# Performance work log

Measured on AMD Instinct MI355X. Metric: run time of the kernel, lower is better.

Reference implementation:

```python
import jax, jax.numpy as jnp
import numpy as np

MULT_CLASS = 6  # int(1/0.2) + 1
EPS = 1e-4


def setup_inputs() -> dict:
    key = jax.random.key(0)
    ks = jax.random.split(key, 8)
    bs, C, M, D = 16384, 10000, MULT_CLASS, 256
    return {
        "data": jax.random.normal(ks[0], (bs, D), dtype=jnp.float32),
        "source_labels": jax.random.randint(ks[1], (bs,), 0, C, dtype=jnp.int32),
        "beta": jax.random.uniform(ks[2], (bs,), dtype=jnp.float32),
        "centers": jax.random.normal(ks[3], (C * M, D), dtype=jnp.float32),
        "W1": jax.random.normal(ks[4], (M, C), dtype=jnp.float32) * 0.02,
        "b1": jnp.zeros((M,), dtype=jnp.float32),
        "W2": jax.random.normal(ks[5], (M, M), dtype=jnp.float32) * 0.1,
        "b2": jnp.zeros((M,), dtype=jnp.float32),
        "memory": jnp.zeros((C * M, D), dtype=jnp.float32),
        "memory_weights": jnp.zeros((C * M, 1), dtype=jnp.float32),
    }


def _weights_from_hotmatrix(beta, labels, W1, b1, W2, b2):
    # LSM(one_hot(label)) : one_hot @ W1.T == gather of W1 columns (same math,
    # avoids materializing the [bs, num_classes] one-hot matrix)
    h = jax.nn.relu(W1.T[labels] + b1)            # [bs, M]
    out = jax.nn.sigmoid(h @ W2.T + b2) + EPS      # [bs, M]
    column_sum = jnp.cumsum(out, axis=1)           # [bs, M]
    val = (beta[:, None] - column_sum) ** 2
    w = jnp.exp(-jnp.sqrt(val + 1e-10))
    norm_w = w / (jnp.sum(w, axis=1, keepdims=True) + EPS + 1e-10)
    return norm_w, column_sum


def reference(data, source_labels, beta, centers, W1, b1, W2, b2, memory, memory_weights):
    bs, D = data.shape
    M = W1.shape[0]
    C = W1.shape[1]
    norm_w, sum_v = _weights_from_hotmatrix(beta, source_labels, W1, b1, W2, b2)

    # --- get_MSML_loss: label-indexed gather of a contiguous center block,
    # per-row weighting, reduce over the block ---
    centers3 = centers.reshape(C, M, D)
    centers_lab = centers3[source_labels]                      # [bs, M, D]
    center_matrix = jnp.einsum("bmd,bm->bd", centers_lab, norm_w)
    loss = jnp.mean((data - center_matrix) ** 2)

    # --- update_center: scatter-add weighted features into memory banks ---
    feat_cent = data[:, None, :] * norm_w[:, :, None]          # [bs, M, D]
    new_memory = memory.reshape(C, M, D).at[source_labels].add(feat_cent)
    new_memory_w = memory_weights.reshape(C, M).at[source_labels].add(norm_w)
    return (loss, sum_v, new_memory.reshape(C * M, D), new_memory_w.reshape(C * M, 1))
```

## Files before the change

kernel.cpp:

```cpp
#include <hip/hip_runtime.h>

constexpr int kBS = 16384;
constexpr int kC  = 10000;
constexpr int kM  = 6;
constexpr int kD  = 256;
constexpr float kEPS = 1e-4f;

__global__ __launch_bounds__(256) void k_build(
    const int* __restrict__ labels,
    int*       head,
    int* __restrict__ next,
    float*     loss_out)
{
    const int row = blockIdx.x * 256 + threadIdx.x;
    if (row == 0) *loss_out = 0.f;
    if (row < kBS) {
        const int lab = labels[row];
        next[row] = atomicExch(head + lab, row);
    }
}

__global__ __launch_bounds__(256) void k_agg(
    const float* __restrict__ data,
    const float* __restrict__ beta,
    const int*   __restrict__ head,
    const int*   __restrict__ next,
    const float* __restrict__ W1,
    const float* __restrict__ b1,
    const float* __restrict__ W2,
    const float* __restrict__ b2,
    const float* __restrict__ centers,
    const float* __restrict__ memory,
    const float* __restrict__ memw,
    float*       loss_out,
    float* __restrict__ sum_v,
    float* __restrict__ mem_out,
    float* __restrict__ mw_out)
{
    __shared__ float ls[4];
    const int wid  = threadIdx.x >> 6;
    const int lane = threadIdx.x & 63;
    const int lab  = blockIdx.x * 4 + wid;

    const size_t cbase = (size_t)lab * (kM * kD);

    float4 cv[kM], mv[kM];
#pragma unroll
    for (int m = 0; m < kM; ++m) {
        cv[m] = ((const float4*)(centers + cbase + (size_t)m * kD))[lane];
        mv[m] = ((const float4*)(memory  + cbase + (size_t)m * kD))[lane];
    }

    float csarr[kM];
    {
        float h[kM];
#pragma unroll
        for (int m = 0; m < kM; ++m) {
            float v = W1[m * kC + lab] + b1[m];
            h[m] = v > 0.f ? v : 0.f;
        }
        float cs = 0.f;
#pragma unroll
        for (int m = 0; m < kM; ++m) {
            float z = b2[m];
#pragma unroll
            for (int j = 0; j < kM; ++j) z += W2[m * kM + j] * h[j];
            cs += 1.f / (1.f + expf(-z)) + kEPS;
            csarr[m] = cs;
        }
    }
    float csel = csarr[0];
    csel = (lane == 1) ? csarr[1] : csel;
    csel = (lane == 2) ? csarr[2] : csel;
    csel = (lane == 3) ? csarr[3] : csel;
    csel = (lane == 4) ? csarr[4] : csel;
    csel = (lane == 5) ? csarr[5] : csel;

    float4 acc[kM];
    float  mwacc[kM];
#pragma unroll
    for (int m = 0; m < kM; ++m) {
        acc[m] = make_float4(0.f, 0.f, 0.f, 0.f);
        mwacc[m] = 0.f;
    }
    float lossacc = 0.f;

    int row = head[lab];
    while (row >= 0) {
        int rows[4];
        int cnt = 0;
        while (row >= 0 && cnt < 4) { rows[cnt++] = row; row = next[row]; }

        float4 dv[4];
        float  bet[4];
#pragma unroll
        for (int i = 0; i < 4; ++i) if (i < cnt) {
            dv[i]  = ((const float4*)(data + (size_t)rows[i] * kD))[lane];
            bet[i] = beta[rows[i]];
        }

#pragma unroll
        for (int i = 0; i < 4; ++i) if (i < cnt) {
            float nw[kM];
            float wsum = 0.f;
#pragma unroll
            for (int m = 0; m < kM; ++m) {
                const float dvb = bet[i] - csarr[m];
                const float wv = expf(-sqrtf(dvb * dvb + 1e-10f));
                nw[m] = wv;
                wsum += wv;
            }
            const float inv = 1.f / (wsum + kEPS + 1e-10f);
            float4 cm = make_float4(0.f, 0.f, 0.f, 0.f);
#pragma unroll
            for (int m = 0; m < kM; ++m) {
                const float w = nw[m] * inv;
                cm.x += w * cv[m].x; cm.y += w * cv[m].y;
                cm.z += w * cv[m].z; cm.w += w * cv[m].w;
                acc[m].x += w * dv[i].x; acc[m].y += w * dv[i].y;
                acc[m].z += w * dv[i].z; acc[m].w += w * dv[i].w;
                mwacc[m] += w;
            }
            const float ax = dv[i].x - cm.x, ay = dv[i].y - cm.y;
            const float az = dv[i].z - cm.z, aw = dv[i].w - cm.w;
            lossacc += ax * ax + ay * ay + az * az + aw * aw;
            if (lane < kM) sum_v[rows[i] * kM + lane] = csel;
        }
    }

#pragma unroll
    for (int m = 0; m < kM; ++m) {
        float4 o;
        o.x = mv[m].x + acc[m].x; o.y = mv[m].y + acc[m].y;
        o.z = mv[m].z + acc[m].z; o.w = mv[m].w + acc[m].w;
        ((float4*)(mem_out + cbase + (size_t)m * kD))[lane] = o;
    }
    float msel = mwacc[0];
    msel = (lane == 1) ? mwacc[1] : msel;
    msel = (lane == 2) ? mwacc[2] : msel;
    msel = (lane == 3) ? mwacc[3] : msel;
    msel = (lane == 4) ? mwacc[4] : msel;
    msel = (lane == 5) ? mwacc[5] : msel;
    if (lane < kM) {
        const size_t i = (size_t)lab * kM + lane;
        mw_out[i] = memw[i] + msel;
    }

#pragma unroll
    for (int off = 32; off > 0; off >>= 1) lossacc += __shfl_down(lossacc, off, 64);
    if (lane == 0) ls[wid] = lossacc;
    __syncthreads();
    if (threadIdx.x == 0) {
        const float s = ls[0] + ls[1] + ls[2] + ls[3];
        atomicAdd(loss_out, s * (1.f / ((float)kBS * (float)kD)));
    }
}

extern "C" void kernel_launch(void* const* d_in, const int* in_sizes, int n_in,
                              void* d_out, int out_size, void* d_ws, size_t ws_size,
                              hipStream_t stream) {
    const float* data    = (const float*)d_in[0];
    const int*   labels  = (const int*)  d_in[1];
    const float* beta    = (const float*)d_in[2];
    const float* centers = (const float*)d_in[3];
    const float* W1      = (const float*)d_in[4];
    const float* b1      = (const float*)d_in[5];
    const float* W2      = (const float*)d_in[6];
    const float* b2      = (const float*)d_in[7];
    const float* memory  = (const float*)d_in[8];
    const float* memw    = (const float*)d_in[9];

    float* out     = (float*)d_out;
    float* loss    = out;
    float* sum_v   = out + 1;
    float* mem_out = out + 1 + (size_t)kBS * kM;
    float* mw_out  = mem_out + (size_t)kC * kM * kD;

    int* head = (int*)d_ws;
    int* next = head + kC;

    hipMemsetAsync(head, 0xFF, kC * sizeof(int), stream);

    k_build<<<dim3((kBS + 255) / 256), dim3(256), 0, stream>>>(
        labels, head, next, loss);

    k_agg<<<dim3(kC / 4), dim3(256), 0, stream>>>(
        data, beta, head, next, W1, b1, W2, b2,
        centers, memory, memw, loss, sum_v, mem_out, mw_out);
}
```

Baseline: 203.9 us.

## Replace linked-list row grouping with counting-sort CSR and skip empty labels

Rows are now bucketed per label with a histogram, a single-block prefix scan and a placement pass, giving a contiguous order array instead of a per-label linked list. The aggregation kernel then reads row indices in batches without serial pointer chasing. It also skips loading centers and computing the label weights for labels with no rows. The cost is two extra kernel launches, including a serial 1024-thread scan.

```diff
diff --git a/kernel.cpp b/kernel.cpp
--- a/kernel.cpp
+++ b/kernel.cpp
@@ -6,25 +6,60 @@
 constexpr int kD  = 256;
 constexpr float kEPS = 1e-4f;
 
-__global__ __launch_bounds__(256) void k_build(
-    const int* __restrict__ labels,
-    int*       head,
-    int* __restrict__ next,
-    float*     loss_out)
+__global__ __launch_bounds__(256) void k_hist(
+    const int* __restrict__ labels, int* counts, int* __restrict__ rank,
+    float* loss_out)
 {
     const int row = blockIdx.x * 256 + threadIdx.x;
     if (row == 0) *loss_out = 0.f;
-    if (row < kBS) {
-        const int lab = labels[row];
-        next[row] = atomicExch(head + lab, row);
-    }
+    if (row < kBS) rank[row] = atomicAdd(counts + labels[row], 1);
+}
+
+__global__ __launch_bounds__(1024) void k_scan(
+    const int* __restrict__ counts, int* __restrict__ starts)
+{
+    __shared__ int part[1024];
+    const int t = threadIdx.x;
+    const int base = t * 10;
+    int local[10];
+    int s = 0;
+#pragma unroll
+    for (int i = 0; i < 10; ++i) {
+        const int idx = base + i;
+        const int c = (idx < kC) ? counts[idx] : 0;
+        local[i] = s; s += c;
+    }
+    part[t] = s;
+    __syncthreads();
+    for (int off = 1; off < 1024; off <<= 1) {
+        const int v = part[t];
+        const int add = (t >= off) ? part[t - off] : 0;
+        __syncthreads();
+        part[t] = v + add;
+        __syncthreads();
+    }
+    const int excl = part[t] - s;
+#pragma unroll
+    for (int i = 0; i < 10; ++i) {
+        const int idx = base + i;
+        if (idx < kC) starts[idx] = excl + local[i];
+    }
+    if (t == 1023) starts[kC] = excl + s;
+}
+
+__global__ __launch_bounds__(256) void k_place(
+    const int* __restrict__ labels, const int* __restrict__ rank,
+    const int* __restrict__ starts, int* __restrict__ order)
+{
+    const int row = blockIdx.x * 256 + threadIdx.x;
+    if (row < kBS) order[starts[labels[row]] + rank[row]] = row;
 }
 
 __global__ __launch_bounds__(256) void k_agg(
     const float* __restrict__ data,
     const float* __restrict__ beta,
-    const int*   __restrict__ head,
-    const int*   __restrict__ next,
+    const int*   __restrict__ starts,
+    const int*   __restrict__ order,
     const float* __restrict__ W1,
     const float* __restrict__ b1,
     const float* __restrict__ W2,
@@ -44,37 +79,8 @@
 
     const size_t cbase = (size_t)lab * (kM * kD);
 
-    float4 cv[kM], mv[kM];
-#pragma unroll
-    for (int m = 0; m < kM; ++m) {
-        cv[m] = ((const float4*)(centers + cbase + (size_t)m * kD))[lane];
-        mv[m] = ((const float4*)(memory  + cbase + (size_t)m * kD))[lane];
-    }
-
-    float csarr[kM];
-    {
-        float h[kM];
-#pragma unroll
-        for (int m = 0; m < kM; ++m) {
-            float v = W1[m * kC + lab] + b1[m];
-            h[m] = v > 0.f ? v : 0.f;
-        }
-        float cs = 0.f;
-#pragma unroll
-        for (int m = 0; m < kM; ++m) {
-            float z = b2[m];
-#pragma unroll
-            for (int j = 0; j < kM; ++j) z += W2[m * kM + j] * h[j];
-            cs += 1.f / (1.f + expf(-z)) + kEPS;
-            csarr[m] = cs;
-        }
-    }
-    float csel = csarr[0];
-    csel = (lane == 1) ? csarr[1] : csel;
-    csel = (lane == 2) ? csarr[2] : csel;
-    csel = (lane == 3) ? csarr[3] : csel;
-    csel = (lane == 4) ? csarr[4] : csel;
-    csel = (lane == 5) ? csarr[5] : csel;
+    const int s0 = starts[lab];
+    const int s1 = starts[lab + 1];
 
     float4 acc[kM];
     float  mwacc[kM];
@@ -85,48 +91,86 @@
     }
     float lossacc = 0.f;
 
-    int row = head[lab];
-    while (row >= 0) {
-        int rows[4];
-        int cnt = 0;
-        while (row >= 0 && cnt < 4) { rows[cnt++] = row; row = next[row]; }
-
-        float4 dv[4];
-        float  bet[4];
-#pragma unroll
-        for (int i = 0; i < 4; ++i) if (i < cnt) {
-            dv[i]  = ((const float4*)(data + (size_t)rows[i] * kD))[lane];
-            bet[i] = beta[rows[i]];
+    if (s1 > s0) {
+        float4 cv[kM];
+#pragma unroll
+        for (int m = 0; m < kM; ++m)
+            cv[m] = ((const float4*)(centers + cbase + (size_t)m * kD))[lane];
+
+        float csarr[kM];
+        {
+            float h[kM];
+#pragma unroll
+            for (int m = 0; m < kM; ++m) {
+                float v = W1[m * kC + lab] + b1[m];
+                h[m] = v > 0.f ? v : 0.f;
+            }
+            float cs = 0.f;
+#pragma unroll
+            for (int m = 0; m < kM; ++m) {
+                float z = b2[m];
+#pragma unroll
+                for (int j = 0; j < kM; ++j) z += W2[m * kM + j] * h[j];
+                cs += 1.f / (1.f + expf(-z)) + kEPS;
+                csarr[m] = cs;
+            }
         }
-
-#pragma unroll
-        for (int i = 0; i < 4; ++i) if (i < cnt) {
-            float nw[kM];
-            float wsum = 0.f;
-#pragma unroll
-            for (int m = 0; m < kM; ++m) {
-                const float dvb = bet[i] - csarr[m];
-                const float wv = expf(-sqrtf(dvb * dvb + 1e-10f));
-                nw[m] = wv;
-                wsum += wv;
-            }
-            const float inv = 1.f / (wsum + kEPS + 1e-10f);
-            float4 cm = make_float4(0.f, 0.f, 0.f, 0.f);
-#pragma unroll
-            for (int m = 0; m < kM; ++m) {
-                const float w = nw[m] * inv;
-                cm.x += w * cv[m].x; cm.y += w * cv[m].y;
-                cm.z += w * cv[m].z; cm.w += w * cv[m].w;
-                acc[m].x += w * dv[i].x; acc[m].y += w * dv[i].y;
-                acc[m].z += w * dv[i].z; acc[m].w += w * dv[i].w;
-                mwacc[m] += w;
-            }
-            const float ax = dv[i].x - cm.x, ay = dv[i].y - cm.y;
-            const float az = dv[i].z - cm.z, aw = dv[i].w - cm.w;
-            lossacc += ax * ax + ay * ay + az * az + aw * aw;
-            if (lane < kM) sum_v[rows[i] * kM + lane] = csel;
+        float csel = csarr[0];
+        csel = (lane == 1) ? csarr[1] : csel;
+        csel = (lane == 2) ? csarr[2] : csel;
+        csel = (lane == 3) ? csarr[3] : csel;
+        csel = (lane == 4) ? csarr[4] : csel;
+        csel = (lane == 5) ? csarr[5] : csel;
+
+        int p = s0;
+        while (p < s1) {
+            const int bc = min(4, s1 - p);
+            int rows[4];
+#pragma unroll
+            for (int i = 0; i < 4; ++i) if (i < bc) rows[i] = order[p + i];
+            float4 dv[4];
+            float  bet[4];
+#pragma unroll
+            for (int i = 0; i < 4; ++i) if (i < bc) {
+                dv[i]  = ((const float4*)(data + (size_t)rows[i] * kD))[lane];
+                bet[i] = beta[rows[i]];
+            }
+#pragma unroll
+            for (int i = 0; i < 4; ++i) if (i < bc) {
+                float nw[kM];
+                float wsum = 0.f;
+#pragma unroll
+                for (int m = 0; m < kM; ++m) {
+                    const float dvb = bet[i] - csarr[m];
+                    const float wv = expf(-sqrtf(dvb * dvb + 1e-10f));
+                    nw[m] = wv;
+                    wsum += wv;
+                }
+                const float inv = 1.f / (wsum + kEPS + 1e-10f);
+                float4 cm = make_float4(0.f, 0.f, 0.f, 0.f);
+#pragma unroll
+                for (int m = 0; m < kM; ++m) {
+                    const float w = nw[m] * inv;
+                    cm.x += w * cv[m].x; cm.y += w * cv[m].y;
+                    cm.z += w * cv[m].z; cm.w += w * cv[m].w;
+                    acc[m].x += w * dv[i].x; acc[m].y += w * dv[i].y;
+                    acc[m].z += w * dv[i].z; acc[m].w += w * dv[i].w;
+                    mwacc[m] += w;
+                }
+                const float ax = dv[i].x - cm.x, ay = dv[i].y - cm.y;
+                const float az = dv[i].z - cm.z, aw = dv[i].w - cm.w;
+                lossacc += ax * ax + ay * ay + az * az + aw * aw;
+                if (lane < kM) sum_v[rows[i] * kM + lane] = csel;
+            }
+            p += bc;
         }
     }
+
+    float4 mv[kM];
+#pragma unroll
+    for (int m = 0; m < kM; ++m)
+        mv[m] = ((const float4*)(memory + cbase + (size_t)m * kD))[lane];
+    const float mwold = (lane < kM) ? memw[(size_t)lab * kM + lane] : 0.f;
 
 #pragma unroll
     for (int m = 0; m < kM; ++m) {
@@ -141,10 +185,7 @@
     msel = (lane == 3) ? mwacc[3] : msel;
     msel = (lane == 4) ? mwacc[4] : msel;
     msel = (lane == 5) ? mwacc[5] : msel;
-    if (lane < kM) {
-        const size_t i = (size_t)lab * kM + lane;
-        mw_out[i] = memw[i] + msel;
-    }
+    if (lane < kM) mw_out[(size_t)lab * kM + lane] = mwold + msel;
 
 #pragma unroll
     for (int off = 32; off > 0; off >>= 1) lossacc += __shfl_down(lossacc, off, 64);
@@ -176,15 +217,22 @@
     float* mem_out = out + 1 + (size_t)kBS * kM;
     float* mw_out  = mem_out + (size_t)kC * kM * kD;
 
-    int* head = (int*)d_ws;
-    int* next = head + kC;
-
-    hipMemsetAsync(head, 0xFF, kC * sizeof(int), stream);
-
-    k_build<<<dim3((kBS + 255) / 256), dim3(256), 0, stream>>>(
-        labels, head, next, loss);
+    int* counts = (int*)d_ws;
+    int* starts = counts + kC;
+    int* rank   = starts + kC + 1;
+    int* order  = rank + kBS;
+
+    hipMemsetAsync(counts, 0, kC * sizeof(int), stream);
+
+    k_hist<<<dim3((kBS + 255) / 256), dim3(256), 0, stream>>>(
+        labels, counts, rank, loss);
+
+    k_scan<<<dim3(1), dim3(1024), 0, stream>>>(counts, starts);
+
+    k_place<<<dim3((kBS + 255) / 256), dim3(256), 0, stream>>>(
+        labels, rank, starts, order);
 
     k_agg<<<dim3(kC / 4), dim3(256), 0, stream>>>(
-        data, beta, head, next, W1, b1, W2, b2,
+        data, beta, starts, order, W1, b1, W2, b2,
         centers, memory, memw, loss, sum_v, mem_out, mw_out);
 }
```

Result: slower. 215.8 us (+5.8%).
